# Optimization experiments

Hardware: AMD Instinct MI355X
Metric: run time of the kernel (lower is better)

## Reference

```python
import jax, jax.numpy as jnp
import numpy as np

HID = 1024
NH = 4  # heads for GAT conv1 and all attention blocks
FF = 2048
SLOPE = 0.2


def _ln(x, g, b):
    m = x.mean(-1, keepdims=True)
    v = ((x - m) ** 2).mean(-1, keepdims=True)
    return (x - m) / jnp.sqrt(v + 1e-5) * g + b


def _mha(q, k, v, in_w, in_b, out_w, out_b, nh):
    # q:[B,Lq,E], k/v:[B,Lk,E]; torch MultiheadAttention math (eval mode)
    B, Lq, E = q.shape
    hd = E // nh
    wq, wk, wv = jnp.split(in_w, 3, axis=0)
    bq, bk, bv = jnp.split(in_b, 3)
    qh = (q @ wq.T + bq).reshape(B, Lq, nh, hd)
    kh = (k @ wk.T + bk).reshape(B, -1, nh, hd)
    vh = (v @ wv.T + bv).reshape(B, -1, nh, hd)
    s = jnp.einsum('bqhd,bkhd->bhqk', qh, kh) / jnp.sqrt(jnp.asarray(hd, q.dtype))
    a = jax.nn.softmax(s, axis=-1)
    o = jnp.einsum('bhqk,bkhd->bqhd', a, vh).reshape(B, Lq, E)
    return o @ out_w.T + out_b


def _gatv2(x, edge_index, w_l, b_l, w_r, b_r, att, bias, heads, out_ch):
    # PyG GATv2Conv, flow='target_to_source': i (aggregation dst) = edge_index[0], j = edge_index[1]
    n = x.shape[0]
    dst = edge_index[0]
    src = edge_index[1]
    x_l = (x @ w_l + b_l).reshape(n, heads, out_ch)
    x_r = (x @ w_r + b_r).reshape(n, heads, out_ch)
    msg = x_l[src]                                   # [E,H,C] gathered source features
    e = jax.nn.leaky_relu(msg + x_r[dst], SLOPE)     # [E,H,C]
    alpha = (e * att).sum(-1)                        # [E,H]
    amax = jax.ops.segment_max(alpha, dst, num_segments=n)
    alpha = jnp.exp(alpha - amax[dst])
    denom = jax.ops.segment_sum(alpha, dst, num_segments=n)
    alpha = alpha / (denom[dst] + 1e-16)
    out = jax.ops.segment_sum(msg * alpha[..., None], dst, num_segments=n)
    return out.reshape(n, heads * out_ch) + bias


def setup_inputs() -> dict:
    key = jax.random.key(0)
    ks = iter(jax.random.split(key, 64))
    N, DF, B, L, E_rand = 8000, 768, 32, 14, 96000
    w = lambda *s: jax.random.normal(next(ks), s, jnp.float32) * 0.02
    z = lambda *s: jnp.zeros(s, jnp.float32)
    o = lambda *s: jnp.ones(s, jnp.float32)
    ei = jax.random.randint(next(ks), (2, E_rand), 0, N, jnp.int32)
    self_loops = jnp.tile(jnp.arange(N, dtype=jnp.int32)[None, :], (2, 1))
    inp = {
        'img_feat': jax.random.normal(next(ks), (B, HID), jnp.float32),
        'node_features': jax.random.normal(next(ks), (N, DF), jnp.float32),
        'edge_index': jnp.concatenate([ei, self_loops], axis=1),
        'target_idx': jax.random.randint(next(ks), (L,), 0, N, jnp.int32),
        # GATv2 conv1: 768 -> 4 heads x 256
        'gat1_wl': w(DF, HID), 'gat1_bl': z(HID), 'gat1_wr': w(DF, HID), 'gat1_br': z(HID),
        'gat1_att': w(NH, HID // NH), 'gat1_bias': z(HID),
        # GATv2 conv2: 1024 -> 1 head x 1024
        'gat2_wl': w(HID, HID), 'gat2_bl': z(HID), 'gat2_wr': w(HID, HID), 'gat2_br': z(HID),
        'gat2_att': w(1, HID), 'gat2_bias': z(HID),
        # cross-modal MHA + FFN layer
        'xa_in_w': w(3 * HID, HID), 'xa_in_b': z(3 * HID), 'xa_out_w': w(HID, HID), 'xa_out_b': z(HID),
        'xl_l1_w': w(FF, HID), 'xl_l1_b': z(FF), 'xl_l2_w': w(HID, FF), 'xl_l2_b': z(HID),
        'xl_n1_g': o(HID), 'xl_n1_b': z(HID), 'xl_n2_g': o(HID), 'xl_n2_b': z(HID),
        # 2-layer TransformerEncoder (stacked leading dim = layer)
        'enc_in_w': w(2, 3 * HID, HID), 'enc_in_b': z(2, 3 * HID),
        'enc_out_w': w(2, HID, HID), 'enc_out_b': z(2, HID),
        'enc_l1_w': w(2, FF, HID), 'enc_l1_b': z(2, FF),
        'enc_l2_w': w(2, HID, FF), 'enc_l2_b': z(2, HID),
        'enc_n1_g': o(2, HID), 'enc_n1_b': z(2, HID),
        'enc_n2_g': o(2, HID), 'enc_n2_b': z(2, HID),
        'cls_w': w(1, HID), 'cls_b': z(1),
    }
    return inp


def reference(img_feat, node_features, edge_index, target_idx,
              gat1_wl, gat1_bl, gat1_wr, gat1_br, gat1_att, gat1_bias,
              gat2_wl, gat2_bl, gat2_wr, gat2_br, gat2_att, gat2_bias,
              xa_in_w, xa_in_b, xa_out_w, xa_out_b,
              xl_l1_w, xl_l1_b, xl_l2_w, xl_l2_b, xl_n1_g, xl_n1_b, xl_n2_g, xl_n2_b,
              enc_in_w, enc_in_b, enc_out_w, enc_out_b, enc_l1_w, enc_l1_b, enc_l2_w, enc_l2_b,
              enc_n1_g, enc_n1_b, enc_n2_g, enc_n2_b, cls_w, cls_b):
    x = _gatv2(node_features, edge_index, gat1_wl, gat1_bl, gat1_wr, gat1_br, gat1_att, gat1_bias, NH, HID // NH)
    x = jax.nn.leaky_relu(x, SLOPE)
    x = _gatv2(x, edge_index, gat2_wl, gat2_bl, gat2_wr, gat2_br, gat2_att, gat2_bias, 1, HID)
    t = x[target_idx]                                  # [L, HID]
    B = img_feat.shape[0]
    L = t.shape[0]
    q = jnp.broadcast_to(t[None], (B, L, HID))
    kv = img_feat[:, None, :]                          # [B, 1, HID]
    attn = _mha(q, kv, kv, xa_in_w, xa_in_b, xa_out_w, xa_out_b, NH)
    src = _ln(t[None] + attn, xl_n1_g, xl_n1_b)
    ff = jax.nn.relu(src @ xl_l1_w.T + xl_l1_b) @ xl_l2_w.T + xl_l2_b
    src = _ln(src + ff, xl_n2_g, xl_n2_b)
    for i in range(2):  # TransformerEncoder, post-norm, relu, eval mode
        a = _mha(src, src, src, enc_in_w[i], enc_in_b[i], enc_out_w[i], enc_out_b[i], NH)
        src = _ln(src + a, enc_n1_g[i], enc_n1_b[i])
        f = jax.nn.relu(src @ enc_l1_w[i].T + enc_l1_b[i]) @ enc_l2_w[i].T + enc_l2_b[i]
        src = _ln(src + f, enc_n2_g[i], enc_n2_b[i])
    return (src @ cls_w.T + cls_b)[..., 0]             # [B, L]
```

## Files before the change

### kernel.cpp

```cpp
#include <hip/hip_runtime.h>
#include <hip/hip_bf16.h>

typedef __bf16 bf16;
typedef bf16 bf16x8 __attribute__((ext_vector_type(8)));
typedef bf16 bf16x4 __attribute__((ext_vector_type(4)));
typedef float f32x4 __attribute__((ext_vector_type(4)));

#define HID 1024
#define FFD 2048
#define DEGCAP 256
#define ROWCAP 16

typedef __attribute__((address_space(3))) void lds_void;
typedef const __attribute__((address_space(1))) void gm_void;

__device__ __forceinline__ void gload_lds16(const bf16* g, bf16* l)
{
    __builtin_amdgcn_global_load_lds((gm_void*)g, (lds_void*)l, 16, 0, 0);
}

__global__ __launch_bounds__(256) void cvt_bf16_kernel(
    const float* __restrict__ src, bf16* __restrict__ dst, long n)
{
    long i = ((long)blockIdx.x * 256 + threadIdx.x) * 4;
    if (i >= n) return;
    float4 f = *(const float4*)&src[i];
    bf16x4 v = {(bf16)f.x, (bf16)f.y, (bf16)f.z, (bf16)f.w};
    *(bf16x4*)&dst[i] = v;
}

__global__ __launch_bounds__(256) void cvt_t_bf16_kernel(
    const float* __restrict__ in, bf16* __restrict__ out, int R, int C)
{
    __shared__ bf16 tile[32][33];
    const int c0 = blockIdx.x * 32, r0 = blockIdx.y * 32;
    const int tx = threadIdx.x & 31, ty = threadIdx.x >> 5;
#pragma unroll
    for (int i = ty; i < 32; i += 8)
        tile[i][tx] = (bf16)in[(long)(r0 + i) * C + c0 + tx];
    __syncthreads();
#pragma unroll
    for (int i = ty; i < 32; i += 8)
        out[(long)(c0 + i) * R + r0 + tx] = tile[tx][i];
}

template <int ACT, int OUTBF16>
__global__ __launch_bounds__(256) void gemm_bf16_kernel(
    const bf16* __restrict__ A, const bf16* __restrict__ B,
    const float* __restrict__ bias, void* __restrict__ Cp,
    int M, int N, int K, int NB)
{
    const int total = gridDim.x;
    const int h = blockIdx.x;
    const int t = (total % 8 == 0) ? ((h & 7) * (total >> 3) + (h >> 3)) : h;
    const int bn = t % NB, bm = t / NB;

    const int tid  = threadIdx.x;
    const int lane = tid & 63, wave = tid >> 6;
    const int wr   = wave >> 1, wc = wave & 1;

    __shared__ bf16 As[128][32];
    __shared__ bf16 Bs[128][32];

    f32x4 acc[4][4] = {};

    const int srow = wave * 16 + (lane >> 2);
    const int scol = (lane & 3) << 3;
    const long ga0 = (long)min(bm * 128 + srow,      M - 1) * K + scol;
    const long ga1 = (long)min(bm * 128 + srow + 64, M - 1) * K + scol;
    const long gb0 = (long)(bn * 128 + srow)      * K + scol;
    const long gb1 = (long)(bn * 128 + srow + 64) * K + scol;
    bf16* ldsA0 = &As[0][0] + wave * 512;
    bf16* ldsA1 = &As[0][0] + 2048 + wave * 512;
    bf16* ldsB0 = &Bs[0][0] + wave * 512;
    bf16* ldsB1 = &Bs[0][0] + 2048 + wave * 512;

    const int quad = lane >> 4;
    const int mr   = lane & 15;
    const int kf   = quad * 8;

    for (int k0 = 0; k0 < K; k0 += 32) {
        gload_lds16(A + ga0 + k0, ldsA0);
        gload_lds16(A + ga1 + k0, ldsA1);
        gload_lds16(B + gb0 + k0, ldsB0);
        gload_lds16(B + gb1 + k0, ldsB1);
        __syncthreads();

        bf16x8 af[4], bfr[4];
#pragma unroll
        for (int i = 0; i < 4; ++i) af[i]  = *(const bf16x8*)&As[wr * 64 + i * 16 + mr][kf];
#pragma unroll
        for (int j = 0; j < 4; ++j) bfr[j] = *(const bf16x8*)&Bs[wc * 64 + j * 16 + mr][kf];
#pragma unroll
        for (int i = 0; i < 4; ++i)
#pragma unroll
            for (int j = 0; j < 4; ++j)
                acc[i][j] = __builtin_amdgcn_mfma_f32_16x16x32_bf16(af[i], bfr[j], acc[i][j], 0, 0, 0);
        __syncthreads();
    }

    const int crow = quad * 4;
#pragma unroll
    for (int i = 0; i < 4; ++i) {
#pragma unroll
        for (int j = 0; j < 4; ++j) {
            const int   col = bn * 128 + wc * 64 + j * 16 + mr;
            const float bv  = bias[col];
#pragma unroll
            for (int r = 0; r < 4; ++r) {
                const int row = bm * 128 + wr * 64 + i * 16 + crow + r;
                if (row < M) {
                    float v = acc[i][j][r] + bv;
                    if (ACT == 1) v = fmaxf(v, 0.f);
                    if (OUTBF16) ((bf16*)Cp)[(long)row * N + col] = (bf16)v;
                    else         ((float*)Cp)[(long)row * N + col] = v;
                }
            }
        }
    }
}

template <int KS>
__global__ __launch_bounds__(256) void gemm_sk_kernel(
    const float* __restrict__ A, const float* __restrict__ Bt,
    float* __restrict__ part, int M, int N, int K)
{
    const int tid  = threadIdx.x;
    const int bn   = blockIdx.x, bm = blockIdx.y, kz = blockIdx.z;
    const int lane = tid & 63, wave = tid >> 6;
    const int wr   = wave >> 1, wc = wave & 1;

    __shared__ bf16 As[128][40];
    __shared__ bf16 Bs[128][40];

    f32x4 acc[4][4] = {};

    const int  lr = tid >> 2;
    const int  lc = (tid & 3) << 3;
    const long a0 = (long)min(bm * 128 + lr,      M - 1) * K;
    const long a1 = (long)min(bm * 128 + lr + 64, M - 1) * K;
    const long b0 = (long)(bn * 128 + lr)      * K;
    const long b1 = (long)(bn * 128 + lr + 64) * K;

    const int quad = lane >> 4;
    const int mr   = lane & 15;
    const int kf   = quad * 8;

    const int Kc   = K / KS;
    const int kbeg = kz * Kc, kend = kbeg + Kc;

    float4 ra[4], rb[4];
    auto load_chunk = [&](int k0) {
        ra[0] = *(const float4*)&A[a0 + k0 + lc];
        ra[1] = *(const float4*)&A[a0 + k0 + lc + 4];
        ra[2] = *(const float4*)&A[a1 + k0 + lc];
        ra[3] = *(const float4*)&A[a1 + k0 + lc + 4];
        rb[0] = *(const float4*)&Bt[b0 + k0 + lc];
        rb[1] = *(const float4*)&Bt[b0 + k0 + lc + 4];
        rb[2] = *(const float4*)&Bt[b1 + k0 + lc];
        rb[3] = *(const float4*)&Bt[b1 + k0 + lc + 4];
    };

    load_chunk(kbeg);
    for (int k0 = kbeg; k0 < kend; k0 += 32) {
        {
            bf16x8 v0 = {(bf16)ra[0].x,(bf16)ra[0].y,(bf16)ra[0].z,(bf16)ra[0].w,
                         (bf16)ra[1].x,(bf16)ra[1].y,(bf16)ra[1].z,(bf16)ra[1].w};
            *(bf16x8*)&As[lr][lc] = v0;
            bf16x8 v1 = {(bf16)ra[2].x,(bf16)ra[2].y,(bf16)ra[2].z,(bf16)ra[2].w,
                         (bf16)ra[3].x,(bf16)ra[3].y,(bf16)ra[3].z,(bf16)ra[3].w};
            *(bf16x8*)&As[lr + 64][lc] = v1;
            bf16x8 v2 = {(bf16)rb[0].x,(bf16)rb[0].y,(bf16)rb[0].z,(bf16)rb[0].w,
                         (bf16)rb[1].x,(bf16)rb[1].y,(bf16)rb[1].z,(bf16)rb[1].w};
            *(bf16x8*)&Bs[lr][lc] = v2;
            bf16x8 v3 = {(bf16)rb[2].x,(bf16)rb[2].y,(bf16)rb[2].z,(bf16)rb[2].w,
                         (bf16)rb[3].x,(bf16)rb[3].y,(bf16)rb[3].z,(bf16)rb[3].w};
            *(bf16x8*)&Bs[lr + 64][lc] = v3;
        }
        __syncthreads();
        if (k0 + 32 < kend) load_chunk(k0 + 32);

        bf16x8 af[4], bfr[4];
#pragma unroll
        for (int i = 0; i < 4; ++i) af[i]  = *(const bf16x8*)&As[wr * 64 + i * 16 + mr][kf];
#pragma unroll
        for (int j = 0; j < 4; ++j) bfr[j] = *(const bf16x8*)&Bs[wc * 64 + j * 16 + mr][kf];
#pragma unroll
        for (int i = 0; i < 4; ++i)
#pragma unroll
            for (int j = 0; j < 4; ++j)
                acc[i][j] = __builtin_amdgcn_mfma_f32_16x16x32_bf16(af[i], bfr[j], acc[i][j], 0, 0, 0);
        __syncthreads();
    }

    const int crow = quad * 4;
    float* dst = part + (size_t)kz * M * N;
#pragma unroll
    for (int i = 0; i < 4; ++i) {
#pragma unroll
        for (int j = 0; j < 4; ++j) {
            const int col = bn * 128 + wc * 64 + j * 16 + mr;
#pragma unroll
            for (int r = 0; r < 4; ++r) {
                const int row = bm * 128 + wr * 64 + i * 16 + crow + r;
                if (row < M) dst[(long)row * N + col] = acc[i][j][r];
            }
        }
    }
}

template <int ACT, int KS>
__global__ __launch_bounds__(256) void sk_reduce_kernel(
    const float* __restrict__ part, const float* __restrict__ bias,
    float* __restrict__ C, long MN, int N)
{
    long i = ((long)blockIdx.x * 256 + threadIdx.x) * 4;
    if (i >= MN) return;
    float4 s = *(const float4*)&part[i];
#pragma unroll
    for (int k = 1; k < KS; ++k) {
        float4 p = *(const float4*)&part[(size_t)k * MN + i];
        s.x += p.x; s.y += p.y; s.z += p.z; s.w += p.w;
    }
    const int col = (int)(i % N);
    float4 bv = *(const float4*)&bias[col];
    s.x += bv.x; s.y += bv.y; s.z += bv.z; s.w += bv.w;
    if (ACT) {
        s.x = fmaxf(s.x, 0.f); s.y = fmaxf(s.y, 0.f);
        s.z = fmaxf(s.z, 0.f); s.w = fmaxf(s.w, 0.f);
    }
    *(float4*)&C[i] = s;
}

__device__ __forceinline__ void ln_finish(float v[4], int c0, const float* g,
                                          const float* beta, float* outrow)
{
    float s1 = v[0] + v[1] + v[2] + v[3];
    float s2 = v[0] * v[0] + v[1] * v[1] + v[2] * v[2] + v[3] * v[3];
    __shared__ float red[8];
    for (int o = 32; o; o >>= 1) { s1 += __shfl_down(s1, o); s2 += __shfl_down(s2, o); }
    const int wave = threadIdx.x >> 6, lane = threadIdx.x & 63;
    if (lane == 0) { red[wave] = s1; red[4 + wave] = s2; }
    __syncthreads();
    if (threadIdx.x == 0) {
        red[0] += red[1] + red[2] + red[3];
        red[4] += red[5] + red[6] + red[7];
    }
    __syncthreads();
    const float mean = red[0] * (1.f / HID);
    const float var  = fmaxf(red[4] * (1.f / HID) - mean * mean, 0.f);
    const float rstd = rsqrtf(var + 1e-5f);
#pragma unroll
    for (int k = 0; k < 4; ++k) {
        int c = c0 + k;
        outrow[c] = (v[k] - mean) * rstd * g[c] + beta[c];
    }
}

template <int KS>
__global__ __launch_bounds__(256) void sk_reduce_ln_kernel(
    const float* __restrict__ part, const float* __restrict__ bias,
    float* __restrict__ srcio, const float* __restrict__ g,
    const float* __restrict__ beta, long MN)
{
    const long row = blockIdx.x;
    const int c0 = threadIdx.x * 4;
    const long base = row * HID + c0;
    float4 s = *(const float4*)&part[base];
#pragma unroll
    for (int k = 1; k < KS; ++k) {
        float4 p = *(const float4*)&part[(size_t)k * MN + base];
        s.x += p.x; s.y += p.y; s.z += p.z; s.w += p.w;
    }
    float4 bv = *(const float4*)&bias[c0];
    float4 rv = *(const float4*)&srcio[base];
    float v[4] = {s.x + bv.x + rv.x, s.y + bv.y + rv.y,
                  s.z + bv.z + rv.z, s.w + bv.w + rv.w};
    ln_finish(v, c0, g, beta, srcio + row * HID);
}

__global__ void zero_i32_kernel(int* __restrict__ p, int n)
{
    int i = blockIdx.x * 256 + threadIdx.x;
    if (i < n) p[i] = 0;
}

__global__ void hist_kernel(const int* __restrict__ ei, int E, int* __restrict__ deg)
{
    int e = blockIdx.x * 256 + threadIdx.x;
    if (e < E) atomicAdd(&deg[ei[e]], 1);
}

__global__ void scan_kernel(const int* __restrict__ deg, int* __restrict__ rowstart,
                            int* __restrict__ cursor, int n)
{
    __shared__ int sm[1024];
    __shared__ int carry;
    if (threadIdx.x == 0) carry = 0;
    __syncthreads();
    for (int base = 0; base < n; base += 1024) {
        int i = base + threadIdx.x;
        int v = (i < n) ? deg[i] : 0;
        sm[threadIdx.x] = v;
        __syncthreads();
        for (int off = 1; off < 1024; off <<= 1) {
            int t = (threadIdx.x >= off) ? sm[threadIdx.x - off] : 0;
            __syncthreads();
            sm[threadIdx.x] += t;
            __syncthreads();
        }
        if (i < n) { int ex = carry + sm[threadIdx.x] - v; rowstart[i] = ex; cursor[i] = ex; }
        __syncthreads();
        if (threadIdx.x == 0) carry += sm[1023];
        __syncthreads();
    }
    if (threadIdx.x == 0) rowstart[n] = carry;
}

__global__ void scatter_kernel(const int* __restrict__ ei, int E,
                               int* __restrict__ cursor, int* __restrict__ eidx)
{
    int e = blockIdx.x * 256 + threadIdx.x;
    if (e < E) { int p = atomicAdd(&cursor[ei[e]], 1); eidx[p] = e; }
}

template <int NH, int LRELU, int OUTBF16>
__global__ __launch_bounds__(256) void gat_fused_kernel(
    const bf16* __restrict__ xl, const bf16* __restrict__ xr,
    const float* __restrict__ att,
    const int* __restrict__ ei, const int* __restrict__ rowstart,
    const int* __restrict__ eidx, const float* __restrict__ bias,
    void* __restrict__ outp, int E)
{
    const int n = blockIdx.x;
    const int tid = threadIdx.x, lane = tid & 63, wave = tid >> 6;
    const int rs = rowstart[n];
    int deg = rowstart[n + 1] - rs;
    if (deg > DEGCAP) deg = DEGCAP;

    __shared__ bf16  xr_sm[HID];
    __shared__ bf16  rows_sm[ROWCAP][HID];
    __shared__ int   src_sm[DEGCAP];
    __shared__ float logit_sm[DEGCAP * NH];

    {
        const int c0 = tid * 4;
        *(bf16x4*)&xr_sm[c0] = *(const bf16x4*)&xr[(long)n * HID + c0];
    }
    for (int j = tid; j < deg; j += 256)
        src_sm[j] = ei[E + eidx[rs + j]];
    __syncthreads();

    const int cA = lane * 8, cB = 512 + lane * 8;
    for (int j = wave; j < deg; j += 4) {
        const long base = (long)src_sm[j] * HID;
        bf16x8 a0 = *(const bf16x8*)&xl[base + cA];
        bf16x8 a1 = *(const bf16x8*)&xl[base + cB];
        if (j < ROWCAP) {
            *(bf16x8*)&rows_sm[j][cA] = a0;
            *(bf16x8*)&rows_sm[j][cB] = a1;
        }
        bf16x8 b0 = *(const bf16x8*)&xr_sm[cA];
        bf16x8 b1 = *(const bf16x8*)&xr_sm[cB];
        float4 tA0 = *(const float4*)&att[cA], tA1 = *(const float4*)&att[cA + 4];
        float4 tB0 = *(const float4*)&att[cB], tB1 = *(const float4*)&att[cB + 4];
        float avA[8] = {tA0.x,tA0.y,tA0.z,tA0.w, tA1.x,tA1.y,tA1.z,tA1.w};
        float avB[8] = {tB0.x,tB0.y,tB0.z,tB0.w, tB1.x,tB1.y,tB1.z,tB1.w};
        float accA = 0.f, accB = 0.f;
#pragma unroll
        for (int t = 0; t < 8; ++t) {
            float v = (float)a0[t] + (float)b0[t];
            v = v > 0.f ? v : 0.2f * v;
            accA += v * avA[t];
            float w = (float)a1[t] + (float)b1[t];
            w = w > 0.f ? w : 0.2f * w;
            accB += w * avB[t];
        }
        if (NH == 4) {
#pragma unroll
            for (int o = 1; o < 32; o <<= 1) {
                accA += __shfl_xor(accA, o);
                accB += __shfl_xor(accB, o);
            }
            if (lane == 0)  { logit_sm[j * 4 + 0] = accA; logit_sm[j * 4 + 2] = accB; }
            if (lane == 32) { logit_sm[j * 4 + 1] = accA; logit_sm[j * 4 + 3] = accB; }
        } else {
            float s = accA + accB;
#pragma unroll
            for (int o = 1; o < 64; o <<= 1) s += __shfl_xor(s, o);
            if (lane == 0) logit_sm[j] = s;
        }
    }
    __syncthreads();

    if (wave < NH) {
        float m = -1e30f;
        for (int j = lane; j < deg; j += 64) m = fmaxf(m, logit_sm[j * NH + wave]);
        for (int o = 32; o; o >>= 1) m = fmaxf(m, __shfl_down(m, o));
        m = __shfl(m, 0);
        float s = 0.f;
        for (int j = lane; j < deg; j += 64) s += expf(logit_sm[j * NH + wave] - m);
        for (int o = 32; o; o >>= 1) s += __shfl_down(s, o);
        s = __shfl(s, 0);
        const float dinv = 1.f / (s + 1e-16f);
        for (int j = lane; j < deg; j += 64)
            logit_sm[j * NH + wave] = expf(logit_sm[j * NH + wave] - m) * dinv;
    }
    __syncthreads();

    const int c0 = tid * 4;
    const int hh = (NH == 4) ? (tid >> 6) : 0;
    float a0 = 0, a1 = 0, a2 = 0, a3 = 0;
    const int dlds = deg < ROWCAP ? deg : ROWCAP;
    for (int j = 0; j < dlds; ++j) {
        const float alpha = logit_sm[j * NH + hh];
        bf16x4 mv = *(const bf16x4*)&rows_sm[j][c0];
        a0 += alpha * (float)mv[0]; a1 += alpha * (float)mv[1];
        a2 += alpha * (float)mv[2]; a3 += alpha * (float)mv[3];
    }
    for (int j = ROWCAP; j < deg; ++j) {
        const float alpha = logit_sm[j * NH + hh];
        bf16x4 mv = *(const bf16x4*)&xl[(long)src_sm[j] * HID + c0];
        a0 += alpha * (float)mv[0]; a1 += alpha * (float)mv[1];
        a2 += alpha * (float)mv[2]; a3 += alpha * (float)mv[3];
    }
    float o4[4] = {a0, a1, a2, a3};
#pragma unroll
    for (int k = 0; k < 4; ++k) {
        float v = o4[k] + bias[c0 + k];
        if (LRELU) v = v > 0.f ? v : 0.2f * v;
        if (OUTBF16) ((bf16*)outp)[(long)n * HID + c0 + k] = (bf16)v;
        else         ((float*)outp)[(long)n * HID + c0 + k] = v;
    }
}

__global__ __launch_bounds__(256) void ln_cross_kernel(
    const float* __restrict__ x2, const int* __restrict__ tidx,
    const float* __restrict__ attnb, const float* __restrict__ g,
    const float* __restrict__ beta, float* __restrict__ out, int L)
{
    const int row = blockIdx.x;
    const int b = row / L, l = row - b * L;
    const long tr = (long)tidx[l] * HID, ar = (long)b * HID;
    const int c0 = threadIdx.x * 4;
    float v[4];
#pragma unroll
    for (int k = 0; k < 4; ++k)
        v[k] = x2[tr + c0 + k] + attnb[ar + c0 + k];
    ln_finish(v, c0, g, beta, out + (long)row * HID);
}

__global__ __launch_bounds__(256) void self_attn_kernel(
    const float* __restrict__ qkv, float* __restrict__ out, int L)
{
    const int b = blockIdx.x >> 2, h = blockIdx.x & 3;
    const int tid = threadIdx.x;
    __shared__ float q[16][256], kk[16][256], vv[16][256];
    __shared__ float sc[16][16];
    for (int i = tid; i < L * 256; i += 256) {
        const int l = i >> 8, d = i & 255;
        const long rb = (long)(b * L + l) * 3072 + h * 256 + d;
        q[l][d]  = qkv[rb];
        kk[l][d] = qkv[rb + 1024];
        vv[l][d] = qkv[rb + 2048];
    }
    __syncthreads();
    if (tid < L * L) {
        const int l1 = tid / L, l2 = tid - l1 * L;
        float s = 0.f;
        for (int d = 0; d < 256; ++d) s += q[l1][d] * kk[l2][d];
        sc[l1][l2] = s * 0.0625f;
    }
    __syncthreads();
    if (tid < L) {
        float mx = -1e30f;
        for (int j = 0; j < L; ++j) mx = fmaxf(mx, sc[tid][j]);
        float ssum = 0.f;
        for (int j = 0; j < L; ++j) { float e = expf(sc[tid][j] - mx); sc[tid][j] = e; ssum += e; }
        const float inv = 1.f / ssum;
        for (int j = 0; j < L; ++j) sc[tid][j] *= inv;
    }
    __syncthreads();
    for (int l1 = 0; l1 < L; ++l1) {
        float a = 0.f;
        for (int l2 = 0; l2 < L; ++l2) a += sc[l1][l2] * vv[l2][tid];
        out[(long)(b * L + l1) * HID + h * 256 + tid] = a;
    }
}

__global__ __launch_bounds__(256) void cls_kernel(
    const float* __restrict__ src, const float* __restrict__ w,
    const float* __restrict__ b, float* __restrict__ out, int rows)
{
    const int row = blockIdx.x * 4 + (threadIdx.x >> 6);
    const int lane = threadIdx.x & 63;
    if (row >= rows) return;
    float s = 0.f;
    for (int c = lane; c < HID; c += 64) s += src[(long)row * HID + c] * w[c];
    for (int o = 32; o; o >>= 1) s += __shfl_down(s, o);
    if (lane == 0) out[row] = s + b[0];
}

extern "C" void kernel_launch(void* const* d_in, const int* in_sizes, int n_in,
                              void* d_out, int out_size, void* d_ws, size_t ws_size,
                              hipStream_t stream)
{
    const float* img_feat      = (const float*)d_in[0];
    const float* node_features = (const float*)d_in[1];
    const int*   edge_index    = (const int*)d_in[2];
    const int*   target_idx    = (const int*)d_in[3];
    const float* gat1_wl  = (const float*)d_in[4];
    const float* gat1_bl  = (const float*)d_in[5];
    const float* gat1_wr  = (const float*)d_in[6];
    const float* gat1_br  = (const float*)d_in[7];
    const float* gat1_att = (const float*)d_in[8];
    const float* gat1_bias= (const float*)d_in[9];
    const float* gat2_wl  = (const float*)d_in[10];
    const float* gat2_bl  = (const float*)d_in[11];
    const float* gat2_wr  = (const float*)d_in[12];
    const float* gat2_br  = (const float*)d_in[13];
    const float* gat2_att = (const float*)d_in[14];
    const float* gat2_bias= (const float*)d_in[15];
    const float* xa_in_w  = (const float*)d_in[16];
    const float* xa_in_b  = (const float*)d_in[17];
    const float* xa_out_w = (const float*)d_in[18];
    const float* xa_out_b = (const float*)d_in[19];
    const float* xl_l1_w  = (const float*)d_in[20];
    const float* xl_l1_b  = (const float*)d_in[21];
    const float* xl_l2_w  = (const float*)d_in[22];
    const float* xl_l2_b  = (const float*)d_in[23];
    const float* xl_n1_g  = (const float*)d_in[24];
    const float* xl_n1_b  = (const float*)d_in[25];
    const float* xl_n2_g  = (const float*)d_in[26];
    const float* xl_n2_b  = (const float*)d_in[27];
    const float* enc_in_w = (const float*)d_in[28];
    const float* enc_in_b = (const float*)d_in[29];
    const float* enc_out_w= (const float*)d_in[30];
    const float* enc_out_b= (const float*)d_in[31];
    const float* enc_l1_w = (const float*)d_in[32];
    const float* enc_l1_b = (const float*)d_in[33];
    const float* enc_l2_w = (const float*)d_in[34];
    const float* enc_l2_b = (const float*)d_in[35];
    const float* enc_n1_g = (const float*)d_in[36];
    const float* enc_n1_b = (const float*)d_in[37];
    const float* enc_n2_g = (const float*)d_in[38];
    const float* enc_n2_b = (const float*)d_in[39];
    const float* cls_w    = (const float*)d_in[40];
    const float* cls_b    = (const float*)d_in[41];

    const int DF = in_sizes[4] / HID;
    const int Nn = in_sizes[1] / DF;
    const int E  = in_sizes[2] / 2;
    const int L  = in_sizes[3];
    const int B  = in_sizes[0] / HID;
    const int R  = B * L;

    char* basep = (char*)d_ws;
    size_t off = 0;
    auto alloc = [&](size_t bytes) -> char* {
        char* r = basep + off; off += (bytes + 255) & ~(size_t)255; return r;
    };
    size_t regA_need = 0;
    {
        auto sz = [&](size_t b) { regA_need += (b + 255) & ~(size_t)255; };
        sz((size_t)Nn * DF * 2); sz((size_t)DF * HID * 2); sz((size_t)DF * HID * 2);
        sz((size_t)HID * HID * 2); sz((size_t)HID * HID * 2); sz((size_t)Nn * HID * 2);
    }
    size_t regA_bytes = regA_need > (size_t)Nn * HID * 4 ? regA_need : (size_t)Nn * HID * 4;
    char* regionA = alloc(regA_bytes);
    {
        size_t aoff = 0;
        auto allocA = [&](size_t bytes) -> char* {
            char* r = regionA + aoff; aoff += (bytes + 255) & ~(size_t)255; return r;
        };
        bf16* nfb  = (bf16*)allocA((size_t)Nn * DF * 2);
        bf16* w1lT = (bf16*)allocA((size_t)DF * HID * 2);
        bf16* w1rT = (bf16*)allocA((size_t)DF * HID * 2);
        bf16* w2lT = (bf16*)allocA((size_t)HID * HID * 2);
        bf16* w2rT = (bf16*)allocA((size_t)HID * HID * 2);
        bf16* x1   = (bf16*)allocA((size_t)Nn * HID * 2);

        float* x2  = (float*)regionA;

        bf16* xlb = (bf16*)alloc((size_t)Nn * HID * 2);
        bf16* xrb = (bf16*)alloc((size_t)Nn * HID * 2);
        int*   deg      = (int*)alloc((size_t)Nn * 4);
        int*   rowstart = (int*)alloc((size_t)(Nn + 1) * 4);
        int*   cursor   = (int*)alloc((size_t)(Nn + 1) * 4);
        int*   eidx     = (int*)alloc((size_t)E * 4);
        float* skpart   = (float*)alloc((size_t)8 * R * 3 * HID * 4);

        char* qb = (char*)xlb; size_t qoff = 0;
        auto alloc2 = [&](size_t bytes) -> char* {
            char* r = qb + qoff; qoff += (bytes + 255) & ~(size_t)255; return r;
        };
        float* vproj  = (float*)alloc2((size_t)B * HID * 4);
        float* attnb  = (float*)alloc2((size_t)B * HID * 4);
        float* srcbuf = (float*)alloc2((size_t)R * HID * 4);
        float* h1buf  = (float*)alloc2((size_t)R * FFD * 4);
        float* ffbuf  = (float*)alloc2((size_t)R * HID * 4);
        float* qkvbuf = (float*)alloc2((size_t)R * 3 * HID * 4);

        const int gE  = (E + 255) / 256;
        const int gMn = (Nn + 127) / 128;
        const long MNr = (long)R * HID;

        auto gemm_sk4 = [&](const float* A, const float* Bt, const float* bias,
                            float* C, int M, int N, int K, int act) {
            gemm_sk_kernel<4><<<dim3(N / 128, (M + 127) / 128, 4), 256, 0, stream>>>(
                A, Bt, skpart, M, N, K);
            long MN = (long)M * N;
            int g = (int)((MN / 4 + 255) / 256);
            if (act) sk_reduce_kernel<1,4><<<g, 256, 0, stream>>>(skpart, bias, C, MN, N);
            else     sk_reduce_kernel<0,4><<<g, 256, 0, stream>>>(skpart, bias, C, MN, N);
        };
        auto gemm_sk8 = [&](const float* A, const float* Bt, const float* bias,
                            float* C, int M, int N, int K, int act) {
            gemm_sk_kernel<8><<<dim3(N / 128, (M + 127) / 128, 8), 256, 0, stream>>>(
                A, Bt, skpart, M, N, K);
            long MN = (long)M * N;
            int g = (int)((MN / 4 + 255) / 256);
            if (act) sk_reduce_kernel<1,8><<<g, 256, 0, stream>>>(skpart, bias, C, MN, N);
            else     sk_reduce_kernel<0,8><<<g, 256, 0, stream>>>(skpart, bias, C, MN, N);
        };
        auto gemm_sk8_ln = [&](const float* A, const float* Bt, const float* bias,
                               float* srcio, const float* g, const float* beta, int K) {
            gemm_sk_kernel<8><<<dim3(HID / 128, (R + 127) / 128, 8), 256, 0, stream>>>(
                A, Bt, skpart, R, HID, K);
            sk_reduce_ln_kernel<8><<<R, 256, 0, stream>>>(skpart, bias, srcio, g, beta, MNr);
        };

        zero_i32_kernel<<<(Nn + 255) / 256, 256, 0, stream>>>(deg, Nn);
        hist_kernel<<<gE, 256, 0, stream>>>(edge_index, E, deg);
        scan_kernel<<<1, 1024, 0, stream>>>(deg, rowstart, cursor, Nn);
        scatter_kernel<<<gE, 256, 0, stream>>>(edge_index, E, cursor, eidx);

        cvt_bf16_kernel<<<(int)(((long)Nn * DF / 4 + 255) / 256), 256, 0, stream>>>(
            node_features, nfb, (long)Nn * DF);
        cvt_t_bf16_kernel<<<dim3(HID / 32, DF / 32), 256, 0, stream>>>(gat1_wl, w1lT, DF, HID);
        cvt_t_bf16_kernel<<<dim3(HID / 32, DF / 32), 256, 0, stream>>>(gat1_wr, w1rT, DF, HID);
        cvt_t_bf16_kernel<<<dim3(HID / 32, HID / 32), 256, 0, stream>>>(gat2_wl, w2lT, HID, HID);
        cvt_t_bf16_kernel<<<dim3(HID / 32, HID / 32), 256, 0, stream>>>(gat2_wr, w2rT, HID, HID);

        gemm_bf16_kernel<0,1><<<8 * gMn, 256, 0, stream>>>(nfb, w1lT, gat1_bl, xlb, Nn, HID, DF, 8);
        gemm_bf16_kernel<0,1><<<8 * gMn, 256, 0, stream>>>(nfb, w1rT, gat1_br, xrb, Nn, HID, DF, 8);
        gat_fused_kernel<4,1,1><<<Nn, 256, 0, stream>>>(xlb, xrb, gat1_att, edge_index,
                                                        rowstart, eidx, gat1_bias, x1, E);

        gemm_bf16_kernel<0,1><<<8 * gMn, 256, 0, stream>>>(x1, w2lT, gat2_bl, xlb, Nn, HID, HID, 8);
        gemm_bf16_kernel<0,1><<<8 * gMn, 256, 0, stream>>>(x1, w2rT, gat2_br, xrb, Nn, HID, HID, 8);
        gat_fused_kernel<1,0,0><<<Nn, 256, 0, stream>>>(xlb, xrb, gat2_att, edge_index,
                                                        rowstart, eidx, gat2_bias, x2, E);

        gemm_sk8(img_feat, xa_in_w + (size_t)2 * HID * HID, xa_in_b + 2 * HID, vproj, B, HID, HID, 0);
        gemm_sk8(vproj, xa_out_w, xa_out_b, attnb, B, HID, HID, 0);
        ln_cross_kernel<<<R, 256, 0, stream>>>(x2, target_idx, attnb, xl_n1_g, xl_n1_b, srcbuf, L);

        gemm_sk4(srcbuf, xl_l1_w, xl_l1_b, h1buf, R, FFD, HID, 1);
        gemm_sk8_ln(h1buf, xl_l2_w, xl_l2_b, srcbuf, xl_n2_g, xl_n2_b, FFD);

        for (int i = 0; i < 2; ++i) {
            gemm_sk4(srcbuf, enc_in_w + (size_t)i * 3 * HID * HID, enc_in_b + i * 3 * HID,
                     qkvbuf, R, 3 * HID, HID, 0);
            self_attn_kernel<<<B * 4, 256, 0, stream>>>(qkvbuf, ffbuf, L);
            gemm_sk8_ln(ffbuf, enc_out_w + (size_t)i * HID * HID, enc_out_b + i * HID,
                        srcbuf, enc_n1_g + i * HID, enc_n1_b + i * HID, HID);
            gemm_sk4(srcbuf, enc_l1_w + (size_t)i * FFD * HID, enc_l1_b + i * FFD,
                     h1buf, R, FFD, HID, 1);
            gemm_sk8_ln(h1buf, enc_l2_w + (size_t)i * HID * FFD, enc_l2_b + i * HID,
                        srcbuf, enc_n2_g + i * HID, enc_n2_b + i * HID, FFD);
        }

        cls_kernel<<<(R + 3) / 4, 256, 0, stream>>>(srcbuf, cls_w, cls_b, (float*)d_out, R);
    }
}
```

Before: 724.6 us.

## Rewrite GAT aggregation as one wave per node with online softmax

The block-per-node GAT kernel, with its LDS staging, separate softmax pass and two block barriers, is replaced by a kernel that gives each node one wave. The wave reads every neighbour row once, computes the logit, and updates an online-softmax running max, sum and weighted accumulator in registers, prefetching the next row. This removes the second global read of neighbour rows past the LDS cap, the shared memory and the syncs, and it packs four nodes per block. The degree cap drops from 256 to 128, which could silently truncate high-degree nodes, and the serial per-edge loop lengthens the dependency chain within each wave.

```diff
diff --git a/kernel.cpp b/kernel.cpp
--- a/kernel.cpp
+++ b/kernel.cpp
@@ -8,8 +8,6 @@
 
 #define HID 1024
 #define FFD 2048
-#define DEGCAP 256
-#define ROWCAP 16
 
 typedef __attribute__((address_space(3))) void lds_void;
 typedef const __attribute__((address_space(1))) void gm_void;
@@ -325,112 +323,109 @@
 }
 
 template <int NH, int LRELU, int OUTBF16>
-__global__ __launch_bounds__(256) void gat_fused_kernel(
+__global__ __launch_bounds__(256) void gat_wave_kernel(
     const bf16* __restrict__ xl, const bf16* __restrict__ xr,
     const float* __restrict__ att,
     const int* __restrict__ ei, const int* __restrict__ rowstart,
     const int* __restrict__ eidx, const float* __restrict__ bias,
-    void* __restrict__ outp, int E)
-{
-    const int n = blockIdx.x;
-    const int tid = threadIdx.x, lane = tid & 63, wave = tid >> 6;
+    void* __restrict__ outp, int E, int Nn)
+{
+    const int wave = threadIdx.x >> 6, lane = threadIdx.x & 63;
+    const int n = blockIdx.x * 4 + wave;
+    if (n >= Nn) return;
+
     const int rs = rowstart[n];
     int deg = rowstart[n + 1] - rs;
-    if (deg > DEGCAP) deg = DEGCAP;
-
-    __shared__ bf16  xr_sm[HID];
-    __shared__ bf16  rows_sm[ROWCAP][HID];
-    __shared__ int   src_sm[DEGCAP];
-    __shared__ float logit_sm[DEGCAP * NH];
-
+    if (deg > 128) deg = 128;
+
+    int my_src = ei[E + eidx[min(rs + lane, E - 1)]];
+    int my_src2 = 0;
+    if (deg > 64) my_src2 = ei[E + eidx[min(rs + 64 + lane, E - 1)]];
+
+    const int c0 = lane * 16;
+    float xrf[16], av[16];
     {
-        const int c0 = tid * 4;
-        *(bf16x4*)&xr_sm[c0] = *(const bf16x4*)&xr[(long)n * HID + c0];
-    }
-    for (int j = tid; j < deg; j += 256)
-        src_sm[j] = ei[E + eidx[rs + j]];
-    __syncthreads();
-
-    const int cA = lane * 8, cB = 512 + lane * 8;
-    for (int j = wave; j < deg; j += 4) {
-        const long base = (long)src_sm[j] * HID;
-        bf16x8 a0 = *(const bf16x8*)&xl[base + cA];
-        bf16x8 a1 = *(const bf16x8*)&xl[base + cB];
-        if (j < ROWCAP) {
-            *(bf16x8*)&rows_sm[j][cA] = a0;
-            *(bf16x8*)&rows_sm[j][cB] = a1;
-        }
-        bf16x8 b0 = *(const bf16x8*)&xr_sm[cA];
-        bf16x8 b1 = *(const bf16x8*)&xr_sm[cB];
-        float4 tA0 = *(const float4*)&att[cA], tA1 = *(const float4*)&att[cA + 4];
-        float4 tB0 = *(const float4*)&att[cB], tB1 = *(const float4*)&att[cB + 4];
-        float avA[8] = {tA0.x,tA0.y,tA0.z,tA0.w, tA1.x,tA1.y,tA1.z,tA1.w};
-        float avB[8] = {tB0.x,tB0.y,tB0.z,tB0.w, tB1.x,tB1.y,tB1.z,tB1.w};
-        float accA = 0.f, accB = 0.f;
-#pragma unroll
-        for (int t = 0; t < 8; ++t) {
-            float v = (float)a0[t] + (float)b0[t];
+        bf16x8 r0 = *(const bf16x8*)&xr[(long)n * HID + c0];
+        bf16x8 r1 = *(const bf16x8*)&xr[(long)n * HID + c0 + 8];
+#pragma unroll
+        for (int t = 0; t < 8; ++t) { xrf[t] = (float)r0[t]; xrf[8 + t] = (float)r1[t]; }
+        float4 t0 = *(const float4*)&att[c0],     t1 = *(const float4*)&att[c0 + 4];
+        float4 t2 = *(const float4*)&att[c0 + 8], t3 = *(const float4*)&att[c0 + 12];
+        av[0]=t0.x; av[1]=t0.y; av[2]=t0.z;  av[3]=t0.w;
+        av[4]=t1.x; av[5]=t1.y; av[6]=t1.z;  av[7]=t1.w;
+        av[8]=t2.x; av[9]=t2.y; av[10]=t2.z; av[11]=t2.w;
+        av[12]=t3.x; av[13]=t3.y; av[14]=t3.z; av[15]=t3.w;
+    }
+
+    float m = -1e30f, s = 0.f;
+    float acc[16];
+#pragma unroll
+    for (int t = 0; t < 16; ++t) acc[t] = 0.f;
+
+    int sj = __shfl(my_src, 0);
+    bf16x8 na0 = *(const bf16x8*)&xl[(long)sj * HID + c0];
+    bf16x8 na1 = *(const bf16x8*)&xl[(long)sj * HID + c0 + 8];
+
+    for (int j = 0; j < deg; ++j) {
+        bf16x8 x0 = na0, x1 = na1;
+        if (j + 1 < deg) {
+            int msrc = (j + 1 < 64) ? my_src : my_src2;
+            int sn = __shfl(msrc, (j + 1) & 63);
+            na0 = *(const bf16x8*)&xl[(long)sn * HID + c0];
+            na1 = *(const bf16x8*)&xl[(long)sn * HID + c0 + 8];
+        }
+        float xf[16];
+#pragma unroll
+        for (int t = 0; t < 8; ++t) { xf[t] = (float)x0[t]; xf[8 + t] = (float)x1[t]; }
+        float partial = 0.f;
+#pragma unroll
+        for (int t = 0; t < 16; ++t) {
+            float v = xf[t] + xrf[t];
             v = v > 0.f ? v : 0.2f * v;
-            accA += v * avA[t];
-            float w = (float)a1[t] + (float)b1[t];
-            w = w > 0.f ? w : 0.2f * w;
-            accB += w * avB[t];
-        }
-        if (NH == 4) {
-#pragma unroll
-            for (int o = 1; o < 32; o <<= 1) {
-                accA += __shfl_xor(accA, o);
-                accB += __shfl_xor(accB, o);
-            }
-            if (lane == 0)  { logit_sm[j * 4 + 0] = accA; logit_sm[j * 4 + 2] = accB; }
-            if (lane == 32) { logit_sm[j * 4 + 1] = accA; logit_sm[j * 4 + 3] = accB; }
-        } else {
-            float s = accA + accB;
-#pragma unroll
-            for (int o = 1; o < 64; o <<= 1) s += __shfl_xor(s, o);
-            if (lane == 0) logit_sm[j] = s;
-        }
-    }
-    __syncthreads();
-
-    if (wave < NH) {
-        float m = -1e30f;
-        for (int j = lane; j < deg; j += 64) m = fmaxf(m, logit_sm[j * NH + wave]);
-        for (int o = 32; o; o >>= 1) m = fmaxf(m, __shfl_down(m, o));
-        m = __shfl(m, 0);
-        float s = 0.f;
-        for (int j = lane; j < deg; j += 64) s += expf(logit_sm[j * NH + wave] - m);
-        for (int o = 32; o; o >>= 1) s += __shfl_down(s, o);
-        s = __shfl(s, 0);
-        const float dinv = 1.f / (s + 1e-16f);
-        for (int j = lane; j < deg; j += 64)
-            logit_sm[j * NH + wave] = expf(logit_sm[j * NH + wave] - m) * dinv;
-    }
-    __syncthreads();
-
-    const int c0 = tid * 4;
-    const int hh = (NH == 4) ? (tid >> 6) : 0;
-    float a0 = 0, a1 = 0, a2 = 0, a3 = 0;
-    const int dlds = deg < ROWCAP ? deg : ROWCAP;
-    for (int j = 0; j < dlds; ++j) {
-        const float alpha = logit_sm[j * NH + hh];
-        bf16x4 mv = *(const bf16x4*)&rows_sm[j][c0];
-        a0 += alpha * (float)mv[0]; a1 += alpha * (float)mv[1];
-        a2 += alpha * (float)mv[2]; a3 += alpha * (float)mv[3];
-    }
-    for (int j = ROWCAP; j < deg; ++j) {
-        const float alpha = logit_sm[j * NH + hh];
-        bf16x4 mv = *(const bf16x4*)&xl[(long)src_sm[j] * HID + c0];
-        a0 += alpha * (float)mv[0]; a1 += alpha * (float)mv[1];
-        a2 += alpha * (float)mv[2]; a3 += alpha * (float)mv[3];
-    }
-    float o4[4] = {a0, a1, a2, a3};
-#pragma unroll
-    for (int k = 0; k < 4; ++k) {
-        float v = o4[k] + bias[c0 + k];
+            partial += v * av[t];
+        }
+        const int RW = (NH == 4) ? 16 : 64;
+#pragma unroll
+        for (int o = 1; o < RW; o <<= 1) partial += __shfl_xor(partial, o);
+        float mn = fmaxf(m, partial);
+        float f = __expf(m - mn);
+        float p = __expf(partial - mn);
+        s = s * f + p;
+#pragma unroll
+        for (int t = 0; t < 16; ++t) acc[t] = acc[t] * f + p * xf[t];
+        m = mn;
+    }
+
+    const float dinv = 1.f / (s + 1e-16f);
+    float bv[16];
+    {
+        float4 t0 = *(const float4*)&bias[c0],     t1 = *(const float4*)&bias[c0 + 4];
+        float4 t2 = *(const float4*)&bias[c0 + 8], t3 = *(const float4*)&bias[c0 + 12];
+        bv[0]=t0.x; bv[1]=t0.y; bv[2]=t0.z;  bv[3]=t0.w;
+        bv[4]=t1.x; bv[5]=t1.y; bv[6]=t1.z;  bv[7]=t1.w;
+        bv[8]=t2.x; bv[9]=t2.y; bv[10]=t2.z; bv[11]=t2.w;
+        bv[12]=t3.x; bv[13]=t3.y; bv[14]=t3.z; bv[15]=t3.w;
+    }
+    float ov[16];
+#pragma unroll
+    for (int t = 0; t < 16; ++t) {
+        float v = acc[t] * dinv + bv[t];
         if (LRELU) v = v > 0.f ? v : 0.2f * v;
-        if (OUTBF16) ((bf16*)outp)[(long)n * HID + c0 + k] = (bf16)v;
-        else         ((float*)outp)[(long)n * HID + c0 + k] = v;
+        ov[t] = v;
+    }
+    if (OUTBF16) {
+        bf16x8 w0, w1;
+#pragma unroll
+        for (int t = 0; t < 8; ++t) { w0[t] = (bf16)ov[t]; w1[t] = (bf16)ov[8 + t]; }
+        *(bf16x8*)&((bf16*)outp)[(long)n * HID + c0] = w0;
+        *(bf16x8*)&((bf16*)outp)[(long)n * HID + c0 + 8] = w1;
+    } else {
+        float* op = (float*)outp + (long)n * HID + c0;
+#pragma unroll
+        for (int t = 0; t < 4; ++t) {
+            float4 w = {ov[t * 4], ov[t * 4 + 1], ov[t * 4 + 2], ov[t * 4 + 3]};
+            *(float4*)&op[t * 4] = w;
+        }
     }
 }
 
@@ -644,13 +639,13 @@
 
         gemm_bf16_kernel<0,1><<<8 * gMn, 256, 0, stream>>>(nfb, w1lT, gat1_bl, xlb, Nn, HID, DF, 8);
         gemm_bf16_kernel<0,1><<<8 * gMn, 256, 0, stream>>>(nfb, w1rT, gat1_br, xrb, Nn, HID, DF, 8);
-        gat_fused_kernel<4,1,1><<<Nn, 256, 0, stream>>>(xlb, xrb, gat1_att, edge_index,
-                                                        rowstart, eidx, gat1_bias, x1, E);
+        gat_wave_kernel<4,1,1><<<(Nn + 3) / 4, 256, 0, stream>>>(
+            xlb, xrb, gat1_att, edge_index, rowstart, eidx, gat1_bias, x1, E, Nn);
 
         gemm_bf16_kernel<0,1><<<8 * gMn, 256, 0, stream>>>(x1, w2lT, gat2_bl, xlb, Nn, HID, HID, 8);
         gemm_bf16_kernel<0,1><<<8 * gMn, 256, 0, stream>>>(x1, w2rT, gat2_br, xrb, Nn, HID, HID, 8);
-        gat_fused_kernel<1,0,0><<<Nn, 256, 0, stream>>>(xlb, xrb, gat2_att, edge_index,
-                                                        rowstart, eidx, gat2_bias, x2, E);
+        gat_wave_kernel<1,0,0><<<(Nn + 3) / 4, 256, 0, stream>>>(
+            xlb, xrb, gat2_att, edge_index, rowstart, eidx, gat2_bias, x2, E, Nn);
 
         gemm_sk8(img_feat, xa_in_w + (size_t)2 * HID * HID, xa_in_b + 2 * HID, vproj, B, HID, HID, 0);
         gemm_sk8(vproj, xa_out_w, xa_out_b, attnb, B, HID, HID, 0);
```

Result: faster. 696.3 us (-3.9%).
